# Kernel optimization log

Measured on AMD Instinct MI355X. Metric: run time of the kernel, lower is better.

## Reference

```python
import jax, jax.numpy as jnp
import numpy as np

BETA = 1.0  # inverse temperature (default of retrieve())
EPS = 1e-12  # matches torch F.normalize eps


def _l2_normalize(x):
    # torch.nn.functional.normalize(p=2, dim=-1): x / max(||x||, eps)
    n = jnp.sqrt(jnp.sum(x * x, axis=-1, keepdims=True))
    return x / jnp.maximum(n, EPS)


def setup_inputs() -> dict:
    key = jax.random.key(0)
    kq, kk = jax.random.split(key)
    N, K, D = 65536, 4096, 128
    queries = jax.random.normal(kq, (N, D), dtype=jnp.float32)
    # learnable memory keys, init_std = 0.02
    keys = jax.random.normal(kk, (K, D), dtype=jnp.float32) * 0.02
    return {"queries": queries, "keys": keys}


def reference(queries, keys):
    # normalize_keys=True, normalize_queries=True
    k_n = _l2_normalize(keys)
    q_n = _l2_normalize(queries)
    # values are TIED to the raw keys parameter (get_values returns self.keys,
    # un-normalized) — only the score-side keys are normalized.
    values = keys
    scores = BETA * jnp.einsum('nd,kd->nk', q_n, k_n)  # [N, K]
    attention = jax.nn.softmax(scores, axis=-1)
    retrieved = jnp.einsum('nk,kd->nd', attention, values)  # [N, D]
    return retrieved
```

## Files before the change

### kernel.cpp

```cpp
#include <hip/hip_runtime.h>
#include <hip/hip_bf16.h>
#include <stdint.h>


typedef __attribute__((ext_vector_type(8))) short bf16x8;
typedef __attribute__((ext_vector_type(16))) float f32x16;

#define MFMA32(a, b, c) __builtin_amdgcn_mfma_f32_32x32x16_bf16(a, b, c, 0, 0, 0)
#define ASYNC_CP16(gsrc, ldst)                                                  \
  __builtin_amdgcn_global_load_lds(                                             \
      (const __attribute__((address_space(1))) void*)(gsrc),                    \
      (__attribute__((address_space(3))) void*)(ldst), 16, 0, 0)

__device__ __forceinline__ unsigned pkbf(float lo, float hi) {
  union { __hip_bfloat162 h2; unsigned u; } v;
  v.h2 = __float22bfloat162_rn(float2{lo, hi});
  return v.u;
}

__global__ __launch_bounds__(256) void prep_k(const float* __restrict__ k,
                                              char* __restrict__ knf,
                                              char* __restrict__ vtf, int K) {
  __shared__ float sRaw[64 * 132];
  __shared__ float sScale[64];
  const int tid = threadIdx.x;
  const int kbase = blockIdx.x * 64;
  {
    const int key_loc = tid >> 2, dq = tid & 3;
    const float4* src = (const float4*)(k + (size_t)(kbase + key_loc) * 128 + dq * 32);
    float4 f[8];
    float ss = 0.f;
#pragma unroll
    for (int i = 0; i < 8; ++i) {
      f[i] = src[i];
      ss += f[i].x * f[i].x + f[i].y * f[i].y + f[i].z * f[i].z + f[i].w * f[i].w;
    }
    ss += __shfl_xor(ss, 1);
    ss += __shfl_xor(ss, 2);
    float4* dst = (float4*)(sRaw + key_loc * 132 + dq * 32);
#pragma unroll
    for (int i = 0; i < 8; ++i) dst[i] = f[i];
    if (dq == 0) sScale[key_loc] = ss > 0.f ? rsqrtf(ss) : 0.f;
  }
  __syncthreads();

#pragma unroll
  for (int r = 0; r < 4; ++r) {
    const int c = r * 256 + tid;
    const int t_loc = c >> 9, ds = (c >> 6) & 7, l = c & 63;
    const int h5 = l >> 5, c32 = l & 31;
    const int key_loc = t_loc * 32 + c32;
    const float sc = sScale[key_loc];
    const float* p = sRaw + key_loc * 132 + ds * 16 + h5 * 8;
    uint4 w;
    w.x = pkbf(p[0] * sc, p[1] * sc);
    w.y = pkbf(p[2] * sc, p[3] * sc);
    w.z = pkbf(p[4] * sc, p[5] * sc);
    w.w = pkbf(p[6] * sc, p[7] * sc);
    *(uint4*)(knf + ((size_t)blockIdx.x * 1024 + c) * 16) = w;
  }
#pragma unroll
  for (int r = 0; r < 4; ++r) {
    const int c = r * 256 + tid;
    const int s = c >> 8, db2 = (c >> 6) & 3, l = c & 63;
    const int h5 = l >> 5, c32 = l & 31;
    const int d = db2 * 32 + c32;
    const int kb = (s >> 1) * 32 + (s & 1) * 8 + h5 * 4;
    float f[8];
#pragma unroll
    for (int j = 0; j < 8; ++j)
      f[j] = sRaw[(kb + (j & 3) + (j >> 2) * 16) * 132 + d];
    uint4 w;
    w.x = pkbf(f[0], f[1]);
    w.y = pkbf(f[2], f[3]);
    w.z = pkbf(f[4], f[5]);
    w.w = pkbf(f[6], f[7]);
    *(uint4*)(vtf + ((size_t)blockIdx.x * 1024 + c) * 16) = w;
  }
}

__global__ __launch_bounds__(256, 2) void attn_main(
    const float* __restrict__ q, const char* __restrict__ knf,
    const char* __restrict__ vtf, float* __restrict__ out, int K) {
  __shared__ __align__(16) char sK[2][16384];
  __shared__ __align__(16) char sV[2][16384];
  const int tid = threadIdx.x;
  const int wave = tid >> 6, lane = tid & 63;
  const int h5 = lane >> 5, c32 = lane & 31;
  const int qrow0 = blockIdx.x * 128 + wave * 32;

  bf16x8 qf[8];
  {
    const float* qr = q + (size_t)(qrow0 + c32) * 128;
    float f[64];
    float ss = 0.f;
#pragma unroll
    for (int ds = 0; ds < 8; ++ds) {
      const float4 a = *(const float4*)(qr + ds * 16 + h5 * 8);
      const float4 b = *(const float4*)(qr + ds * 16 + h5 * 8 + 4);
      f[ds * 8 + 0] = a.x; f[ds * 8 + 1] = a.y; f[ds * 8 + 2] = a.z; f[ds * 8 + 3] = a.w;
      f[ds * 8 + 4] = b.x; f[ds * 8 + 5] = b.y; f[ds * 8 + 6] = b.z; f[ds * 8 + 7] = b.w;
    }
#pragma unroll
    for (int i = 0; i < 64; ++i) ss += f[i] * f[i];
    ss += __shfl_xor(ss, 32);
    const float sc = (ss > 0.f ? rsqrtf(ss) : 0.f) * 1.44269504f;
#pragma unroll
    for (int ds = 0; ds < 8; ++ds) {
      union { unsigned u[4]; bf16x8 v; } t;
#pragma unroll
      for (int p = 0; p < 4; ++p)
        t.u[p] = pkbf(f[ds * 8 + 2 * p] * sc, f[ds * 8 + 2 * p + 1] * sc);
      qf[ds] = t.v;
    }
  }

  f32x16 acc[4];
#pragma unroll
  for (int db2 = 0; db2 < 4; ++db2)
#pragma unroll
    for (int r = 0; r < 16; ++r) acc[db2][r] = 0.f;
  float den = 0.f;
  f32x16 Zf;
#pragma unroll
  for (int r = 0; r < 16; ++r) Zf[r] = 0.f;

  union pfu { unsigned u[4]; bf16x8 v; };
  pfu pf[4];
  f32x16 Sa[2], Sb[2];

  const int nIter = K >> 6;

  auto stageK = [&](int it, int buf) {
#pragma unroll
    for (int i = 0; i < 4; ++i)
      ASYNC_CP16(knf + (size_t)it * 16384 + (wave * 4 + i) * 1024 + lane * 16,
                 sK[buf] + (wave * 4 + i) * 1024);
  };
  auto stageV = [&](int it, int buf) {
#pragma unroll
    for (int i = 0; i < 4; ++i)
      ASYNC_CP16(vtf + (size_t)it * 16384 + (wave * 4 + i) * 1024 + lane * 16,
                 sV[buf] + (wave * 4 + i) * 1024);
  };

  auto computeS = [&](int buf, f32x16* S) {
#pragma unroll
    for (int t = 0; t < 2; ++t) {
      f32x16 s;
#pragma unroll
      for (int ds = 0; ds < 8; ++ds) {
        const bf16x8 kf = *(const bf16x8*)(sK[buf] + (t * 8 + ds) * 1024 + lane * 16);
        s = MFMA32(kf, qf[ds], (ds == 0) ? Zf : s);
      }
      S[t] = s;
    }
  };

  auto doExp = [&](const f32x16* S) {
#pragma unroll
    for (int s = 0; s < 4; ++s) {
      const int t = s >> 1, w = s & 1;
      float e[8];
#pragma unroll
      for (int j = 0; j < 8; ++j) {
        const int rr = w * 4 + (j & 3) + (j >> 2) * 8;
        e[j] = __builtin_amdgcn_exp2f(S[t][rr]);
      }
      den += ((e[0] + e[1]) + (e[2] + e[3])) + ((e[4] + e[5]) + (e[6] + e[7]));
#pragma unroll
      for (int j2 = 0; j2 < 4; ++j2) pf[s].u[j2] = pkbf(e[2 * j2], e[2 * j2 + 1]);
    }
  };

  auto doPV = [&](int buf) {
    const char* vb = sV[buf] + lane * 16;
#pragma unroll
    for (int s = 0; s < 4; ++s) {
      bf16x8 v0 = *(const bf16x8*)(vb + (s * 4 + 0) * 1024);
      bf16x8 v1 = *(const bf16x8*)(vb + (s * 4 + 1) * 1024);
      bf16x8 v2 = *(const bf16x8*)(vb + (s * 4 + 2) * 1024);
      bf16x8 v3 = *(const bf16x8*)(vb + (s * 4 + 3) * 1024);
      acc[0] = MFMA32(v0, pf[s].v, acc[0]);
      acc[1] = MFMA32(v1, pf[s].v, acc[1]);
      acc[2] = MFMA32(v2, pf[s].v, acc[2]);
      acc[3] = MFMA32(v3, pf[s].v, acc[3]);
    }
  };

  stageK(0, 0);
  stageV(0, 0);
  __syncthreads();
  stageK(1, 1);
  computeS(0, Sa);

  __syncthreads();
  stageK(2, 0);
  stageV(1, 1);
  __builtin_amdgcn_s_setprio(1);
  computeS(1, Sb);
  doExp(Sa);
  doPV(0);
  __builtin_amdgcn_s_setprio(0);

  for (int itp = 2; itp < nIter; itp += 2) {
    __syncthreads();
    stageK(itp + 1, 1);
    stageV(itp, 0);
    __builtin_amdgcn_s_setprio(1);
    computeS(0, Sa);
    doExp(Sb);
    doPV(1);
    __builtin_amdgcn_s_setprio(0);

    __syncthreads();
    if (itp + 2 < nIter) stageK(itp + 2, 0);
    stageV(itp + 1, 1);
    __builtin_amdgcn_s_setprio(1);
    computeS(1, Sb);
    doExp(Sa);
    doPV(0);
    __builtin_amdgcn_s_setprio(0);
  }

  __syncthreads();
  doExp(Sb);
  doPV(1);

  den += __shfl_xor(den, 32);
  const float rd = 1.0f / den;

  __syncthreads();
  float* wls = (float*)(&sK[0][0] + wave * 4096);
#pragma unroll
  for (int db2 = 0; db2 < 4; ++db2) {
#pragma unroll
    for (int qd = 0; qd < 4; ++qd) {
      float4 v;
      v.x = acc[db2][qd * 4 + 0] * rd;
      v.y = acc[db2][qd * 4 + 1] * rd;
      v.z = acc[db2][qd * 4 + 2] * rd;
      v.w = acc[db2][qd * 4 + 3] * rd;
      *(float4*)(wls + c32 * 32 + (((h5 + 2 * qd) ^ (c32 & 7)) << 2)) = v;
    }
#pragma unroll
    for (int p = 0; p < 4; ++p) {
      const int ql = p * 8 + (lane >> 3);
      const int x = lane & 7;
      const float4 v = *(const float4*)(wls + ql * 32 + ((x ^ (ql & 7)) << 2));
      *(float4*)(out + (size_t)(qrow0 + ql) * 128 + db2 * 32 + x * 4) = v;
    }
  }
}

extern "C" void kernel_launch(void* const* d_in, const int* in_sizes, int n_in,
                              void* d_out, int out_size, void* d_ws, size_t ws_size,
                              hipStream_t stream) {
  const float* q = (const float*)d_in[0];
  const float* k = (const float*)d_in[1];
  const int N = in_sizes[0] / 128;
  const int K = in_sizes[1] / 128;
  char* ws = (char*)d_ws;
  char* knf = ws;
  char* vtf = ws + (size_t)K * 256;
  float* out = (float*)d_out;

  prep_k<<<dim3(K / 64), dim3(256), 0, stream>>>(k, knf, vtf, K);
  attn_main<<<dim3(N / 128), dim3(256), 0, stream>>>(q, knf, vtf, out, K);
}
```

Measured before the change: 202.3 us.

## Deepen software pipeline so PV lags exp by one tile

Restructures the main loop so the P·V MFMA for a tile runs one stage after its exponentials. Two P fragment buffers (pfA/pfB) are added and V staging is shifted one iteration later. This separates the exp results from their consumer MFMAs and so hides the exp-to-MFMA dependency latency. The cost is extra registers for the second P buffer, which could pressure occupancy at two blocks per CU, plus a longer epilogue with an extra barrier.

```diff
diff --git a/kernel.cpp b/kernel.cpp
--- a/kernel.cpp
+++ b/kernel.cpp
@@ -126,7 +126,7 @@
   for (int r = 0; r < 16; ++r) Zf[r] = 0.f;
 
   union pfu { unsigned u[4]; bf16x8 v; };
-  pfu pf[4];
+  pfu pfA[4], pfB[4];
   f32x16 Sa[2], Sb[2];
 
   const int nIter = K >> 6;
@@ -157,7 +157,7 @@
     }
   };
 
-  auto doExp = [&](const f32x16* S) {
+  auto doExp = [&](const f32x16* S, pfu* pf) {
 #pragma unroll
     for (int s = 0; s < 4; ++s) {
       const int t = s >> 1, w = s & 1;
@@ -173,7 +173,7 @@
     }
   };
 
-  auto doPV = [&](int buf) {
+  auto doPV = [&](int buf, const pfu* pf) {
     const char* vb = sV[buf] + lane * 16;
 #pragma unroll
     for (int s = 0; s < 4; ++s) {
@@ -189,43 +189,43 @@
   };
 
   stageK(0, 0);
-  stageV(0, 0);
   __syncthreads();
   stageK(1, 1);
   computeS(0, Sa);
 
   __syncthreads();
   stageK(2, 0);
-  stageV(1, 1);
+  stageV(0, 0);
   __builtin_amdgcn_s_setprio(1);
   computeS(1, Sb);
-  doExp(Sa);
-  doPV(0);
+  doExp(Sa, pfA);
   __builtin_amdgcn_s_setprio(0);
 
-  for (int itp = 2; itp < nIter; itp += 2) {
+  for (int it = 2; it < nIter; it += 2) {
     __syncthreads();
-    stageK(itp + 1, 1);
-    stageV(itp, 0);
+    stageK(it + 1, 1);
+    stageV(it - 1, 1);
     __builtin_amdgcn_s_setprio(1);
     computeS(0, Sa);
-    doExp(Sb);
-    doPV(1);
+    doExp(Sb, pfB);
+    doPV(0, pfA);
     __builtin_amdgcn_s_setprio(0);
 
     __syncthreads();
-    if (itp + 2 < nIter) stageK(itp + 2, 0);
-    stageV(itp + 1, 1);
+    if (it + 2 < nIter) stageK(it + 2, 0);
+    stageV(it, 0);
     __builtin_amdgcn_s_setprio(1);
     computeS(1, Sb);
-    doExp(Sa);
-    doPV(0);
+    doExp(Sa, pfA);
+    doPV(1, pfB);
     __builtin_amdgcn_s_setprio(0);
   }
-
-  __syncthreads();
-  doExp(Sb);
-  doPV(1);
+  __syncthreads();
+  stageV(nIter - 1, 1);
+  doExp(Sb, pfB);
+  doPV(0, pfA);
+  __syncthreads();
+  doPV(1, pfB);
 
   den += __shfl_xor(den, 32);
   const float rd = 1.0f / den;
```

New measurement: 207.2 us. +2.4%, slower.
